# Performance work log

Measured on AMD Instinct MI355X. Metric: run time of the kernel, lower is better.

## Reference

```python
import jax, jax.numpy as jnp
import numpy as np

B, T, C = 4, 1024, 1024
HEAD_SIZE = 64
H = C // HEAD_SIZE
N_LAYER, LAYER_ID = 24, 12
D_MIX_LORA, D_DECAY_LORA = 32, 64
HEAD_SIZE_DIVISOR = 8
LN_EPS = 1e-5 * HEAD_SIZE_DIVISOR ** 2


def setup_inputs() -> dict:
    key = jax.random.key(0)
    ks = jax.random.split(key, 16)
    x = jax.random.normal(ks[0], (B, T, C), jnp.float32)

    r01 = LAYER_ID / (N_LAYER - 1)          # ratio_0_to_1
    r10 = 1.0 - LAYER_ID / N_LAYER          # ratio_1_to_almost0
    ddd = np.arange(C, dtype=np.float64) / C

    time_maa_x = jnp.asarray((1.0 - ddd ** r10).astype(np.float32))
    time_maa_w = jnp.asarray((1.0 - ddd ** r10).astype(np.float32))
    time_maa_k = jnp.asarray((1.0 - ddd ** r10).astype(np.float32))
    time_maa_v = jnp.asarray((1.0 - (ddd ** r10 + 0.3 * r01)).astype(np.float32))
    time_maa_r = jnp.asarray((1.0 - ddd ** (0.5 * r10)).astype(np.float32))
    time_maa_g = jnp.asarray((1.0 - ddd ** (0.5 * r10)).astype(np.float32))

    n = np.arange(C, dtype=np.float64)
    time_decay = jnp.asarray((-6.0 + 5.0 * (n / (C - 1)) ** (0.7 + 1.3 * r01)).astype(np.float32))
    zigzag = ((n + 1) % 3 - 1) * 0.1
    time_faaaa = jnp.asarray((r01 * (1.0 - n / (C - 1)) + zigzag).astype(np.float32)).reshape(H, HEAD_SIZE)

    u = lambda k, shp: jax.random.uniform(k, shp, jnp.float32, -0.01, 0.01)
    time_maa_w1 = u(ks[1], (C, D_MIX_LORA * 5))   # zeros in orig init; small random for a non-trivial test
    time_maa_w2 = u(ks[2], (5, D_MIX_LORA, C))
    time_decay_w1 = u(ks[3], (C, D_DECAY_LORA))
    time_decay_w2 = u(ks[4], (D_DECAY_LORA, C))

    s = 1.0 / np.sqrt(C)
    Wr = jax.random.normal(ks[5], (C, C), jnp.float32) * s   # stored [in, out]
    Wk = jax.random.normal(ks[6], (C, C), jnp.float32) * s
    Wv = jax.random.normal(ks[7], (C, C), jnp.float32) * s
    Wg = jax.random.normal(ks[8], (C, C), jnp.float32) * s
    Wo = jax.random.normal(ks[9], (C, C), jnp.float32) * s
    ln_w = jnp.ones((C,), jnp.float32)
    ln_b = jnp.zeros((C,), jnp.float32)

    return dict(x=x, time_maa_x=time_maa_x, time_maa_w=time_maa_w, time_maa_k=time_maa_k,
                time_maa_v=time_maa_v, time_maa_r=time_maa_r, time_maa_g=time_maa_g,
                time_maa_w1=time_maa_w1, time_maa_w2=time_maa_w2,
                time_decay=time_decay, time_decay_w1=time_decay_w1, time_decay_w2=time_decay_w2,
                time_faaaa=time_faaaa, Wr=Wr, Wk=Wk, Wv=Wv, Wg=Wg, Wo=Wo, ln_w=ln_w, ln_b=ln_b)


def _wkv6(r, k, v, w, u):
    # r,k,v,w: [B,T,H,N]; u: [H,N]. Data-dependent linear recurrence per head.
    def step(S, inp):               # S: [B,H,N,N] (key dim j, value dim i)
        r_t, k_t, v_t, w_t = inp    # each [B,H,N]
        y = jnp.einsum('bhj,bhji->bhi', r_t, S) \
            + jnp.sum(r_t * u * k_t, axis=-1, keepdims=True) * v_t
        decay = jnp.exp(-jnp.exp(w_t))            # CUDA kernel: w_eff = exp(-exp(w))
        S = decay[..., None] * S + k_t[..., None] * v_t[..., None, :]
        return S, y

    to_t = lambda a: jnp.transpose(a, (1, 0, 2, 3))  # [T,B,H,N]
    S0 = jnp.zeros(r.shape[:1] + (r.shape[2], r.shape[3], r.shape[3]), r.dtype)
    _, ys = jax.lax.scan(step, S0, (to_t(r), to_t(k), to_t(v), to_t(w)))
    return jnp.transpose(ys, (1, 0, 2, 3))            # [B,T,H,N]


def reference(x, time_maa_x, time_maa_w, time_maa_k, time_maa_v, time_maa_r, time_maa_g,
              time_maa_w1, time_maa_w2, time_decay, time_decay_w1, time_decay_w2,
              time_faaaa, Wr, Wk, Wv, Wg, Wo, ln_w, ln_b):
    b, t, c = x.shape
    h, n = H, HEAD_SIZE

    # token shift: ZeroPad2d((0,0,1,-1)) shifts time right by one with zero pad
    xx = jnp.concatenate([jnp.zeros_like(x[:, :1]), x[:, :-1]], axis=1) - x
    xxx = x + xx * time_maa_x
    mix = jnp.tanh(xxx @ time_maa_w1).reshape(b, t, 5, D_MIX_LORA)
    m = jnp.einsum('btsd,sdc->sbtc', mix, time_maa_w2)  # [5,B,T,C]
    xw = x + xx * (time_maa_w + m[0])
    xk = x + xx * (time_maa_k + m[1])
    xv = x + xx * (time_maa_v + m[2])
    xr = x + xx * (time_maa_r + m[3])
    xg = x + xx * (time_maa_g + m[4])

    r = xr @ Wr
    k = xk @ Wk
    v = xv @ Wv
    g = jax.nn.silu(xg @ Wg)
    w = time_decay + jnp.tanh(xw @ time_decay_w1) @ time_decay_w2

    y = _wkv6(r.reshape(b, t, h, n), k.reshape(b, t, h, n),
              v.reshape(b, t, h, n), w.reshape(b, t, h, n), time_faaaa)

    # GroupNorm with n_head groups over channel dim, eps = 1e-5 * divisor^2
    mu = y.mean(-1, keepdims=True)
    var = y.var(-1, keepdims=True)
    yn = ((y - mu) / jnp.sqrt(var + LN_EPS)).reshape(b, t, c) * ln_w + ln_b

    return (yn * g) @ Wo
```

## Files before the change

### kernel.cpp

```cpp
#include <hip/hip_runtime.h>

typedef unsigned short u16;
typedef short short8 __attribute__((ext_vector_type(8)));
typedef short short4v __attribute__((ext_vector_type(4)));
typedef float float4v __attribute__((ext_vector_type(4)));
typedef unsigned uint4v __attribute__((ext_vector_type(4)));

__device__ __forceinline__ float bf2f(u16 h) { return __uint_as_float(((unsigned)h) << 16); }
__device__ __forceinline__ u16 f2bf(float f) {
  unsigned u = __float_as_uint(f);
  unsigned r = (u + 0x7fffu + ((u >> 16) & 1u)) >> 16;
  return (u16)r;
}
__device__ __forceinline__ bool is_f32(const void* probe) {
  return ((const u16*)probe)[0] != 0x3F80;
}
__device__ __forceinline__ float ldin(const void* p, long i, bool f32m) {
  return f32m ? ((const float*)p)[i] : bf2f(((const u16*)p)[i]);
}

typedef __attribute__((address_space(1))) const unsigned int as1_u32;
typedef __attribute__((address_space(3))) unsigned int as3_u32;
__device__ __forceinline__ void gl2lds16(const void* g, void* l) {
  __builtin_amdgcn_global_load_lds((as1_u32*)g, (as3_u32*)l, 16, 0, 0);
}

template <int CTRL>
__device__ __forceinline__ float dpp_add(float x) {
  int s = __builtin_amdgcn_update_dpp(0, __float_as_int(x), CTRL, 0xF, 0xF, true);
  return x + __int_as_float(s);
}

__global__ __launch_bounds__(256) void sentinel_fill(u16* o, long n) {
  long i = (long)blockIdx.x * 256 + threadIdx.x;
  if (i < n) o[i] = 0x42C8;
}

struct TDescArr {
  const void* src[13];
  u16* dst[13];
  int rows[13];
  int cols[13];
  int roff[13];
};

__global__ __launch_bounds__(256) void transpose_all(TDescArr d, const void* probe) {
  bool f32m = is_f32(probe);
  int z = blockIdx.z;
  int rows = d.rows[z], cols = d.cols[z], roff = d.roff[z];
  int bc = blockIdx.x * 32, br = blockIdx.y * 32;
  if (bc >= cols || br >= rows) return;
  const void* src = d.src[z];
  u16* dst = d.dst[z];
  __shared__ u16 tile[32][33];
  int tx = threadIdx.x & 31, ty = threadIdx.x >> 5;
#pragma unroll
  for (int i = 0; i < 32; i += 8)
    tile[ty + i][tx] = f2bf(ldin(src, (long)(roff + br + ty + i) * cols + bc + tx, f32m));
  __syncthreads();
#pragma unroll
  for (int i = 0; i < 32; i += 8)
    dst[(long)(bc + ty + i) * rows + br + tx] = tile[tx][ty + i];
}

__global__ __launch_bounds__(256) void token_shift(const void* __restrict__ x,
                                                   const void* __restrict__ maa_x,
                                                   u16* __restrict__ xxx) {
  bool f32m = is_f32(maa_x);
  long idx = (long)blockIdx.x * 256 + threadIdx.x;
  int c = (int)(idx & 1023);
  int tt = (int)((idx >> 10) & 1023);
  float xv = ldin(x, idx, f32m);
  float xp = tt > 0 ? ldin(x, idx - 1024, f32m) : 0.f;
  xxx[idx] = f2bf(xv + (xp - xv) * ldin(maa_x, c, f32m));
}

template <int EPI>
__device__ __forceinline__ void gemm128_core(const u16* __restrict__ A,
                                             const u16* __restrict__ Bt,
                                             void* __restrict__ Cv, int N, int K,
                                             int m0, int n0, u16* As, u16* Bs,
                                             bool f32m) {
  int t = threadIdx.x, lane = t & 63, w = t >> 6;
  int wm = (w >> 1) * 64, wn = (w & 1) * 64;
  int lr = lane & 15, lk = lane >> 4;
  float4v acc[4][4];
#pragma unroll
  for (int i = 0; i < 4; i++)
#pragma unroll
    for (int j = 0; j < 4; j++) acc[i][j] = (float4v){0.f, 0.f, 0.f, 0.f};
  int srow = t >> 3;
  int scol = ((t & 7) ^ (srow & 7)) * 8;
  const u16* Ag = A + (long)(m0 + srow) * K + scol;
  const u16* Bg = Bt + (long)(n0 + srow) * K + scol;
  int so = w * 512;
  for (int k0 = 0; k0 < K; k0 += 64) {
    __syncthreads();
#pragma unroll
    for (int p = 0; p < 4; p++) {
      gl2lds16(Ag + (long)p * 32 * K + k0, As + p * 2048 + so);
      gl2lds16(Bg + (long)p * 32 * K + k0, Bs + p * 2048 + so);
    }
    __syncthreads();
    short8 af[4][2], bfr[4][2];
#pragma unroll
    for (int i = 0; i < 4; i++) {
      int R = wm + i * 16 + lr;
#pragma unroll
      for (int h = 0; h < 2; h++) {
        int j = h * 4 + lk;
        af[i][h] = *(const short8*)(As + R * 64 + (j ^ (R & 7)) * 8);
      }
    }
#pragma unroll
    for (int i = 0; i < 4; i++) {
      int R = wn + i * 16 + lr;
#pragma unroll
      for (int h = 0; h < 2; h++) {
        int j = h * 4 + lk;
        bfr[i][h] = *(const short8*)(Bs + R * 64 + (j ^ (R & 7)) * 8);
      }
    }
#pragma unroll
    for (int mi2 = 0; mi2 < 4; mi2++)
#pragma unroll
      for (int ni2 = 0; ni2 < 4; ni2++) {
        acc[mi2][ni2] = __builtin_amdgcn_mfma_f32_16x16x32_bf16(
            af[mi2][0], bfr[ni2][0], acc[mi2][ni2], 0, 0, 0);
        acc[mi2][ni2] = __builtin_amdgcn_mfma_f32_16x16x32_bf16(
            af[mi2][1], bfr[ni2][1], acc[mi2][ni2], 0, 0, 0);
      }
  }
#pragma unroll
  for (int mi2 = 0; mi2 < 4; mi2++) {
#pragma unroll
    for (int ni2 = 0; ni2 < 4; ni2++) {
      int col = n0 + wn + ni2 * 16 + lr;
#pragma unroll
      for (int rr = 0; rr < 4; rr++) {
        long row = m0 + wm + mi2 * 16 + lk * 4 + rr;
        float val = acc[mi2][ni2][rr];
        if (EPI == 1) val = val / (1.f + __expf(-val));
        if (EPI == 2 && f32m) ((float*)Cv)[row * N + col] = val;
        else ((u16*)Cv)[row * N + col] = f2bf(val);
      }
    }
  }
}

template <int EPI>
__global__ __launch_bounds__(256, 2) void gemm_big(const u16* __restrict__ A,
                                                   const u16* __restrict__ Bt,
                                                   void* __restrict__ Cv, int M, int N,
                                                   int K, const void* probe) {
  __shared__ alignas(16) u16 As[128 * 64];
  __shared__ alignas(16) u16 Bs[128 * 64];
  int sid = blockIdx.y * gridDim.x + blockIdx.x;
  int per8 = (gridDim.x * gridDim.y) >> 3;
  int L = (sid & 7) * per8 + (sid >> 3);
  int mi = L / gridDim.y, ni = L % gridDim.y;
  bool f32m = (EPI == 2) ? is_f32(probe) : false;
  gemm128_core<EPI>(A, Bt, Cv, N, K, mi * 128, ni * 128, As, Bs, f32m);
}

template <int EPI0, int EPI1>
__global__ __launch_bounds__(256, 2) void gemm_big2(
    const u16* __restrict__ A0, const u16* __restrict__ Bt0, u16* __restrict__ C0,
    const u16* __restrict__ A1, const u16* __restrict__ Bt1, u16* __restrict__ C1,
    int M, int N, int K) {
  __shared__ alignas(16) u16 As[128 * 64];
  __shared__ alignas(16) u16 Bs[128 * 64];
  int z = blockIdx.z;
  int sid = blockIdx.y * gridDim.x + blockIdx.x;
  int per8 = (gridDim.x * gridDim.y) >> 3;
  int L = (sid & 7) * per8 + (sid >> 3);
  int mi = L / gridDim.y, ni = L % gridDim.y;
  if (z == 0)
    gemm128_core<EPI0>(A0, Bt0, C0, N, K, mi * 128, ni * 128, As, Bs, false);
  else
    gemm128_core<EPI1>(A1, Bt1, C1, N, K, mi * 128, ni * 128, As, Bs, false);
}

template <int EPI>
__global__ __launch_bounds__(256) void gemm_wave(const u16* __restrict__ A, int lda,
                                                 const u16* __restrict__ Bt,
                                                 u16* __restrict__ C, int ldc,
                                                 float* dA_, float* dB_, int Ntot,
                                                 int K, const void* aux0,
                                                 const void* probe,
                                                 const void* __restrict__ xin) {
  int t = threadIdx.x, lane = t & 63, w = t >> 6;
  int m0 = blockIdx.x * 64 + w * 16;
  int span = Ntot / gridDim.y;
  int col0 = blockIdx.y * span;
  const u16* Bp = Bt + (long)col0 * K;
  int lr = lane & 15, lk = lane >> 4;
  bool f32m = (EPI >= 2) ? is_f32(probe) : false;
  int nt = span >> 4;
  for (int g0 = 0; g0 < nt; g0 += 4) {
    int gc = (nt - g0 < 4) ? (nt - g0) : 4;
    float4v acc[4];
#pragma unroll
    for (int i = 0; i < 4; i++) acc[i] = (float4v){0.f, 0.f, 0.f, 0.f};
    for (int k0 = 0; k0 < K; k0 += 32) {
      short8 a = *(const short8*)(A + (long)(m0 + lr) * lda + k0 + lk * 8);
      for (int gi = 0; gi < gc; gi++) {
        int n0 = (g0 + gi) * 16;
        short8 b = *(const short8*)(Bp + (long)(n0 + lr) * K + k0 + lk * 8);
        acc[gi] = __builtin_amdgcn_mfma_f32_16x16x32_bf16(a, b, acc[gi], 0, 0, 0);
      }
    }
    for (int gi = 0; gi < gc; gi++) {
      int col = col0 + (g0 + gi) * 16 + lr;
      if (EPI == 3) {
        long r0 = m0 + lk * 4;
        float xv4[4];
#pragma unroll
        for (int rr = 0; rr < 4; rr++)
          xv4[rr] = ldin(xin, (r0 + rr) * 1024 + col, f32m);
        float xpv = ((int)(r0 & 1023) > 0) ? ldin(xin, (r0 - 1) * 1024 + col, f32m) : 0.f;
        float mv = ldin(aux0, col, f32m);
#pragma unroll
        for (int rr = 0; rr < 4; rr++) {
          float xv = xv4[rr];
          float xp = (rr == 0) ? xpv : xv4[rr - 1];
          C[(r0 + rr) * 1024 + col] = f2bf(xv + (xp - xv) * (mv + acc[gi][rr]));
        }
      } else {
#pragma unroll
        for (int rr = 0; rr < 4; rr++) {
          long row = m0 + lk * 4 + rr;
          float val = acc[gi][rr];
          if (EPI == 0) {
            C[row * ldc + col] = f2bf(val);
          } else if (EPI == 1) {
            float vv = fminf(fmaxf(val, -15.f), 15.f);
            float e = __expf(2.f * vv);
            C[row * ldc + col] = f2bf((e - 1.f) / (e + 1.f));
          } else if (EPI == 2) {
            float wv = val + ldin(aux0, col, f32m);
            float ew = __expf(wv);
            if (row < 2048) dA_[row * 1024 + col] = ew;
            else dB_[(row - 2048) * 1024 + col] = ew;
          }
        }
      }
    }
  }
}

__global__ __launch_bounds__(256) void gemm_wave3_pair(
    const u16* __restrict__ A0, const u16* __restrict__ Bt0, u16* __restrict__ C0,
    const void* __restrict__ maa0, const u16* __restrict__ A1,
    const u16* __restrict__ Bt1, u16* __restrict__ C1,
    const void* __restrict__ maa1, const void* probe,
    const void* __restrict__ xin) {
  int z = blockIdx.z;
  const u16* A = z ? A1 : A0;
  const u16* Bt = z ? Bt1 : Bt0;
  u16* C = z ? C1 : C0;
  const void* maa = z ? maa1 : maa0;
  bool f32m = is_f32(probe);
  int t = threadIdx.x, lane = t & 63, w = t >> 6;
  int m0 = blockIdx.x * 64 + w * 16;
  int col0 = blockIdx.y * 32;
  const u16* Bp = Bt + (long)col0 * 32;
  int lr = lane & 15, lk = lane >> 4;
  float4v acc[2];
  acc[0] = (float4v){0.f, 0.f, 0.f, 0.f};
  acc[1] = (float4v){0.f, 0.f, 0.f, 0.f};
  short8 a = *(const short8*)(A + (long)(m0 + lr) * 160 + lk * 8);
#pragma unroll
  for (int gi = 0; gi < 2; gi++) {
    short8 b = *(const short8*)(Bp + (long)(gi * 16 + lr) * 32 + lk * 8);
    acc[gi] = __builtin_amdgcn_mfma_f32_16x16x32_bf16(a, b, acc[gi], 0, 0, 0);
  }
#pragma unroll
  for (int gi = 0; gi < 2; gi++) {
    int col = col0 + gi * 16 + lr;
    long r0 = m0 + lk * 4;
    float xv4[4];
#pragma unroll
    for (int rr = 0; rr < 4; rr++)
      xv4[rr] = ldin(xin, (r0 + rr) * 1024 + col, f32m);
    float xpv = ((int)(r0 & 1023) > 0) ? ldin(xin, (r0 - 1) * 1024 + col, f32m) : 0.f;
    float mv = ldin(maa, col, f32m);
#pragma unroll
    for (int rr = 0; rr < 4; rr++) {
      float xv = xv4[rr];
      float xp = (rr == 0) ? xpv : xv4[rr - 1];
      C[(r0 + rr) * 1024 + col] = f2bf(xv + (xp - xv) * (mv + acc[gi][rr]));
    }
  }
}

__global__ __launch_bounds__(256) void gemm_n64_tanh(const u16* __restrict__ A,
                                                     const u16* __restrict__ Bt,
                                                     u16* __restrict__ C) {
  int t = threadIdx.x, lane = t & 63, w = t >> 6;
  int m0 = blockIdx.x * 16;
  int n0 = w * 16;
  int lr = lane & 15, lk = lane >> 4;
  float4v acc = (float4v){0.f, 0.f, 0.f, 0.f};
  const u16* Ap = A + (long)(m0 + lr) * 1024;
  const u16* Bp = Bt + (long)(n0 + lr) * 1024;
  for (int k0 = 0; k0 < 1024; k0 += 32) {
    short8 a = *(const short8*)(Ap + k0 + lk * 8);
    short8 b = *(const short8*)(Bp + k0 + lk * 8);
    acc = __builtin_amdgcn_mfma_f32_16x16x32_bf16(a, b, acc, 0, 0, 0);
  }
#pragma unroll
  for (int rr = 0; rr < 4; rr++) {
    long row = m0 + lk * 4 + rr;
    float vv = fminf(fmaxf(acc[rr], -15.f), 15.f);
    float e = __expf(2.f * vv);
    C[row * 64 + n0 + lr] = f2bf((e - 1.f) / (e + 1.f));
  }
}

__global__ __launch_bounds__(256) void wkv6_chunk(
    const u16* __restrict__ r, const u16* __restrict__ k, const u16* __restrict__ v,
    const float* __restrict__ ewA, const float* __restrict__ ewB,
    const void* __restrict__ u_, const void* probe, u16* __restrict__ y) {
  bool f32m = is_f32(probe);
  int bx = blockIdx.x;
  int vs = bx >> 6, bh = bx & 63;
  int b = bh >> 4, h = bh & 15;
  int tid = threadIdx.x, lane = tid & 63, w = tid >> 6;
  int lr = lane & 15, lk = lane >> 4;

  __shared__ alignas(16) float raw[32][68];
  __shared__ alignas(16) float scc[2][32][68];
  __shared__ alignas(16) u16 Rp[32][72];
  __shared__ alignas(16) u16 Kp[32][72];
  __shared__ alignas(16) u16 KdF[64 * 40 + 56];
  __shared__ alignas(16) u16 Vt[32][40];
  __shared__ alignas(16) u16 Pb[32][40];
  __shared__ alignas(16) u16 Sh[32][72];
  __shared__ alignas(16) u16 Sl[32][72];
  __shared__ float diag32[32];

  const long base = ((long)b << 20) + h * 64;
  const float* ewg =
      (b < 2 ? ewA + (long)b * 1048576 : ewB + (long)(b - 2) * 1048576) + h * 64;

  int tt = tid >> 3, kg = tid & 7;
  int ck = w * 16 + (lane & 15);
  int cq = lane >> 4;
  float u8[8];
#pragma unroll
  for (int i = 0; i < 8; i++) u8[i] = ldin(u_, h * 64 + kg * 8 + i, f32m);

  float4v Sst[2];
  Sst[0] = (float4v){0.f, 0.f, 0.f, 0.f};
  Sst[1] = (float4v){0.f, 0.f, 0.f, 0.f};
  int skey = w * 16 + lk * 4;

  {
    long grow = (long)tt << 10;
    float4v ewlo = *(const float4v*)(ewg + grow + kg * 8);
    float4v ewhi = *(const float4v*)(ewg + grow + kg * 8 + 4);
    short8 rraw = *(const short8*)(r + base + grow + kg * 8);
    short8 kraw = *(const short8*)(k + base + grow + kg * 8);
    short4v vraw = *(const short4v*)(v + base + grow + vs * 32 + kg * 4);
    *(float4v*)&raw[tt][kg * 8] = ewlo;
    *(float4v*)&raw[tt][kg * 8 + 4] = ewhi;
    __syncthreads();
    {
      float pseg[8];
      float s = 0.f;
#pragma unroll
      for (int j = 0; j < 8; j++) {
        s += raw[cq * 8 + j][ck];
        pseg[j] = s;
      }
      float tot = pseg[7], x = tot;
      float up = __shfl_up(x, 16);
      if (cq >= 1) x += up;
      up = __shfl_up(x, 32);
      if (cq >= 2) x += up;
      float pre = x - tot;
#pragma unroll
      for (int j = 0; j < 8; j++) scc[0][cq * 8 + j][ck] = pre + pseg[j];
    }
    __syncthreads();
    {
      float pd = 0.f;
      short8 rpv, kpv;
#pragma unroll
      for (int i = 0; i < 8; i++) {
        int key = kg * 8 + i;
        float rf = bf2f((u16)rraw[i]);
        float kf = bf2f((u16)kraw[i]);
        float si = scc[0][tt][key];
        float sx = tt ? scc[0][tt - 1][key] : 0.f;
        float sE = scc[0][31][key];
        rpv[i] = (short)f2bf(rf * __expf(-sx));
        kpv[i] = (short)f2bf(kf * __expf(si));
        KdF[key * 40 + ((key >> 3) & 7) * 8 + tt] = f2bf(kf * __expf(si - sE));
        pd = fmaf(rf * u8[i], kf, pd);
      }
      *(short8*)&Rp[tt][kg * 8] = rpv;
      *(short8*)&Kp[tt][kg * 8] = kpv;
      pd = dpp_add<0xB1>(pd);
      pd = dpp_add<0x4E>(pd);
      pd = dpp_add<0x104>(pd);
      if (kg == 0) diag32[tt] = pd;
    }
#pragma unroll
    for (int i = 0; i < 4; i++) Vt[kg * 4 + i][tt] = (u16)vraw[i];
#pragma unroll
    for (int vt = 0; vt < 2; vt++) {
      short4v z4 = (short4v){0, 0, 0, 0};
      *(short4v*)&Sh[lr + vt * 16][skey] = z4;
      *(short4v*)&Sl[lr + vt * 16][skey] = z4;
    }
    __syncthreads();
  }

  for (int ci = 0; ci < 32; ++ci) {
    int c0 = ci << 5;
    int c0n = (ci == 31) ? c0 : c0 + 32;
    int pc = ci & 1, pn = pc ^ 1;
    long grow = (long)(c0n + tt) << 10;
    float4v ewlo = *(const float4v*)(ewg + grow + kg * 8);
    float4v ewhi = *(const float4v*)(ewg + grow + kg * 8 + 4);
    short8 rraw = *(const short8*)(r + base + grow + kg * 8);
    short8 kraw = *(const short8*)(k + base + grow + kg * 8);
    short4v vraw = *(const short4v*)(v + base + grow + vs * 32 + kg * 4);

    {
      int pt = w >> 1, pj = w & 1;
      float4v pacc = (float4v){0.f, 0.f, 0.f, 0.f};
      short8 aP0 = *(const short8*)&Rp[pt * 16 + lr][lk * 8];
      short8 aP1 = *(const short8*)&Rp[pt * 16 + lr][lk * 8 + 32];
      short8 bP0 = *(const short8*)&Kp[pj * 16 + lr][lk * 8];
      short8 bP1 = *(const short8*)&Kp[pj * 16 + lr][lk * 8 + 32];
      pacc = __builtin_amdgcn_mfma_f32_16x16x32_bf16(aP0, bP0, pacc, 0, 0, 0);
      pacc = __builtin_amdgcn_mfma_f32_16x16x32_bf16(aP1, bP1, pacc, 0, 0, 0);
      int jcol = pj * 16 + lr;
#pragma unroll
      for (int rr = 0; rr < 4; rr++) {
        int trow = pt * 16 + lk * 4 + rr;
        float val = (jcol < trow) ? pacc[rr] : (jcol == trow ? diag32[trow] : 0.f);
        Pb[trow][jcol] = f2bf(val);
      }
    }
    *(float4v*)&raw[tt][kg * 8] = ewlo;
    *(float4v*)&raw[tt][kg * 8 + 4] = ewhi;
    __syncthreads();

    {
      float pseg[8];
      float s = 0.f;
#pragma unroll
      for (int j = 0; j < 8; j++) {
        s += raw[cq * 8 + j][ck];
        pseg[j] = s;
      }
      float tot = pseg[7], x = tot;
      float up = __shfl_up(x, 16);
      if (cq >= 1) x += up;
      up = __shfl_up(x, 32);
      if (cq >= 2) x += up;
      float pre = x - tot;
#pragma unroll
      for (int j = 0; j < 8; j++) scc[pn][cq * 8 + j][ck] = pre + pseg[j];
    }
    {
      int yt = w >> 1, yv = w & 1;
      float4v yacc = (float4v){0.f, 0.f, 0.f, 0.f};
      short8 aY = *(const short8*)&Pb[yt * 16 + lr][lk * 8];
      short8 bY = *(const short8*)&Vt[yv * 16 + lr][lk * 8];
      yacc = __builtin_amdgcn_mfma_f32_16x16x32_bf16(aY, bY, yacc, 0, 0, 0);
      short8 aR0 = *(const short8*)&Rp[yt * 16 + lr][lk * 8];
      short8 aR1 = *(const short8*)&Rp[yt * 16 + lr][lk * 8 + 32];
      short8 bH0 = *(const short8*)&Sh[yv * 16 + lr][lk * 8];
      short8 bH1 = *(const short8*)&Sh[yv * 16 + lr][lk * 8 + 32];
      short8 bL0 = *(const short8*)&Sl[yv * 16 + lr][lk * 8];
      short8 bL1 = *(const short8*)&Sl[yv * 16 + lr][lk * 8 + 32];
      yacc = __builtin_amdgcn_mfma_f32_16x16x32_bf16(aR0, bH0, yacc, 0, 0, 0);
      yacc = __builtin_amdgcn_mfma_f32_16x16x32_bf16(aR1, bH1, yacc, 0, 0, 0);
      yacc = __builtin_amdgcn_mfma_f32_16x16x32_bf16(aR0, bL0, yacc, 0, 0, 0);
      yacc = __builtin_amdgcn_mfma_f32_16x16x32_bf16(aR1, bL1, yacc, 0, 0, 0);
#pragma unroll
      for (int rr = 0; rr < 4; rr++) {
        int trow = yt * 16 + lk * 4 + rr;
        y[base + ((long)(c0 + trow) << 10) + vs * 32 + yv * 16 + lr] = f2bf(yacc[rr]);
      }
      int kr = w * 16 + lr;
      short8 aS = *(const short8*)&KdF[kr * 40 + ((kr >> 3) & 7) * 8 + lk * 8];
      short8 bS0 = *(const short8*)&Vt[lr][lk * 8];
      short8 bS1 = *(const short8*)&Vt[16 + lr][lk * 8];
      float4v sa0 = (float4v){0.f, 0.f, 0.f, 0.f};
      float4v sa1 = (float4v){0.f, 0.f, 0.f, 0.f};
      sa0 = __builtin_amdgcn_mfma_f32_16x16x32_bf16(aS, bS0, sa0, 0, 0, 0);
      sa1 = __builtin_amdgcn_mfma_f32_16x16x32_bf16(aS, bS1, sa1, 0, 0, 0);
#pragma unroll
      for (int rr = 0; rr < 4; rr++) {
        float cl = __expf(-scc[pc][31][skey + rr]);
        Sst[0][rr] = fmaf(Sst[0][rr], cl, sa0[rr]);
        Sst[1][rr] = fmaf(Sst[1][rr], cl, sa1[rr]);
      }
    }
    __syncthreads();

    {
      float pd = 0.f;
      short8 rpv, kpv;
#pragma unroll
      for (int i = 0; i < 8; i++) {
        int key = kg * 8 + i;
        float rf = bf2f((u16)rraw[i]);
        float kf = bf2f((u16)kraw[i]);
        float si = scc[pn][tt][key];
        float sx = tt ? scc[pn][tt - 1][key] : 0.f;
        float sE = scc[pn][31][key];
        rpv[i] = (short)f2bf(rf * __expf(-sx));
        kpv[i] = (short)f2bf(kf * __expf(si));
        KdF[key * 40 + ((key >> 3) & 7) * 8 + tt] = f2bf(kf * __expf(si - sE));
        pd = fmaf(rf * u8[i], kf, pd);
      }
      *(short8*)&Rp[tt][kg * 8] = rpv;
      *(short8*)&Kp[tt][kg * 8] = kpv;
      pd = dpp_add<0xB1>(pd);
      pd = dpp_add<0x4E>(pd);
      pd = dpp_add<0x104>(pd);
      if (kg == 0) diag32[tt] = pd;
    }
#pragma unroll
    for (int i = 0; i < 4; i++) Vt[kg * 4 + i][tt] = (u16)vraw[i];
#pragma unroll
    for (int vt = 0; vt < 2; vt++) {
      short4v hi4, lo4;
#pragma unroll
      for (int rr = 0; rr < 4; rr++) {
        u16 hv = f2bf(Sst[vt][rr]);
        hi4[rr] = (short)hv;
        lo4[rr] = (short)f2bf(Sst[vt][rr] - bf2f(hv));
      }
      *(short4v*)&Sh[lr + vt * 16][skey] = hi4;
      *(short4v*)&Sl[lr + vt * 16][skey] = lo4;
    }
    __syncthreads();
  }
}

__global__ __launch_bounds__(256) void gn_gate(const u16* __restrict__ y,
                                               const u16* __restrict__ g,
                                               const void* __restrict__ lnw,
                                               const void* __restrict__ lnb,
                                               const void* probe,
                                               u16* __restrict__ out) {
  bool f32m = is_f32(probe);
  int gid = blockIdx.x * 4 + (threadIdx.x >> 6);
  int lane = threadIdx.x & 63;
  int h = gid & 15;
  long row = gid >> 4;
  long off = row * 1024 + h * 64 + lane;
  float val = bf2f(y[off]);
  float s = val, sq = val * val;
#pragma unroll
  for (int m = 1; m < 64; m <<= 1) {
    s += __shfl_xor(s, m);
    sq += __shfl_xor(sq, m);
  }
  float mean = s * (1.f / 64.f);
  float var = fmaxf(sq * (1.f / 64.f) - mean * mean, 0.f);
  float inv = rsqrtf(var + 6.4e-4f);
  int c = h * 64 + lane;
  float yn = (val - mean) * inv * ldin(lnw, c, f32m) + ldin(lnb, c, f32m);
  out[off] = f2bf(yn * bf2f(g[off]));
}

extern "C" void kernel_launch(void* const* d_in, const int* in_sizes, int n_in,
                              void* d_out, int out_size, void* d_ws, size_t ws_size,
                              hipStream_t stream) {
  const void* x = d_in[0];
  const void* maaX = d_in[1];
  const void* maa_s[5] = {d_in[2], d_in[3], d_in[4], d_in[5], d_in[6]};
  const void* w1 = d_in[7];
  const void* w2 = d_in[8];
  const void* tdec = d_in[9];
  const void* dw1 = d_in[10];
  const void* dw2 = d_in[11];
  const void* faaaa = d_in[12];
  const void* Wr = d_in[13];
  const void* Wk = d_in[14];
  const void* Wv = d_in[15];
  const void* Wg = d_in[16];
  const void* Wo = d_in[17];
  const void* lnw = d_in[18];
  const void* lnb = d_in[19];

  const long oWoT = 4194304;
  const long ow1T = 5242880;
  const long odw1T = 5406720;
  const long odw2T = 5472256;
  const long ow2T = 5537792;
  const long omixb = 5701632;
  const long owtan = 6356992;
  const long oxxxg = 6619136;
  const long omx = 10813440;
  const long orb = 15007744;
  const long okb = 19202048;
  const long ovb = 23396352;
  const long oyb = 27590656;
  const long oend = 31784960;
  const size_t needed = (size_t)oend * 2;

  if (ws_size < needed) {
    sentinel_fill<<<dim3((unsigned)((out_size + 255) / 256)), 256, 0, stream>>>(
        (u16*)d_out, out_size);
    return;
  }

  u16* W = (u16*)d_ws;
  u16* WrT = W;
  u16* WkT = W + 1048576;
  u16* WvT = W + 2097152;
  u16* WgT = W + 3145728;
  u16* WoT = W + oWoT;
  u16* w1T = W + ow1T;
  u16* dw1T = W + odw1T;
  u16* dw2T = W + odw2T;
  u16* w2T = W + ow2T;
  u16* mixb = W + omixb;
  u16* wtan = W + owtan;
  u16* xxxg = W + oxxxg;
  u16* mx = W + omx;
  u16* rbuf = W + orb;
  u16* kbuf = W + okb;
  u16* vbuf = W + ovb;
  u16* ybuf = W + oyb;
  float* dA_ = (float*)W;
  float* dB_ = (float*)(W + omx);
  u16* gated = mx;

  TDescArr td;
  const void* s5[5] = {Wr, Wk, Wv, Wg, Wo};
  u16* t5[5] = {WrT, WkT, WvT, WgT, WoT};
  for (int i = 0; i < 13; i++) td.roff[i] = 0;
  for (int i = 0; i < 5; i++) {
    td.src[i] = s5[i]; td.dst[i] = t5[i]; td.rows[i] = 1024; td.cols[i] = 1024;
  }
  td.src[5] = w1;  td.dst[5] = w1T;  td.rows[5] = 1024; td.cols[5] = 160;
  td.src[6] = dw1; td.dst[6] = dw1T; td.rows[6] = 1024; td.cols[6] = 64;
  td.src[7] = dw2; td.dst[7] = dw2T; td.rows[7] = 64;   td.cols[7] = 1024;
  for (int s = 0; s < 5; s++) {
    td.src[8 + s] = w2;
    td.dst[8 + s] = w2T + s * 1024 * 32;
    td.rows[8 + s] = 32; td.cols[8 + s] = 1024; td.roff[8 + s] = s * 32;
  }

  transpose_all<<<dim3(32, 32, 13), 256, 0, stream>>>(td, maaX);
  token_shift<<<dim3(16384), 256, 0, stream>>>(x, maaX, xxxg);
  gemm_wave<1><<<dim3(64, 10), 256, 0, stream>>>(xxxg, 1024, w1T, mixb, 160, nullptr,
                                                 nullptr, 160, 1024, nullptr, nullptr,
                                                 nullptr);
  gemm_wave3_pair<<<dim3(64, 32, 2), 256, 0, stream>>>(
      mixb + 3 * 32, w2T + 3 * 32768, mx, maa_s[3],
      mixb + 1 * 32, w2T + 1 * 32768, ybuf, maa_s[1], maaX, x);
  gemm_big2<0, 0><<<dim3(32, 8, 2), 256, 0, stream>>>(mx, WrT, rbuf, ybuf, WkT, kbuf,
                                                      4096, 1024, 1024);
  gemm_wave3_pair<<<dim3(64, 32, 2), 256, 0, stream>>>(
      mixb + 2 * 32, w2T + 2 * 32768, mx, maa_s[2],
      mixb + 4 * 32, w2T + 4 * 32768, ybuf, maa_s[4], maaX, x);
  gemm_big2<0, 1><<<dim3(32, 8, 2), 256, 0, stream>>>(mx, WvT, vbuf, ybuf, WgT, xxxg,
                                                      4096, 1024, 1024);
  gemm_wave<3><<<dim3(64, 32), 256, 0, stream>>>(mixb + 0 * 32, 160, w2T + 0 * 32768,
                                                 mx, 1024, nullptr, nullptr, 1024, 32,
                                                 maa_s[0], maaX, x);
  gemm_n64_tanh<<<dim3(256), 256, 0, stream>>>(mx, dw1T, wtan);
  gemm_wave<2><<<dim3(64, 16), 256, 0, stream>>>(wtan, 64, dw2T, nullptr, 0, dA_, dB_,
                                                 1024, 64, tdec, maaX, nullptr);
  wkv6_chunk<<<dim3(128), 256, 0, stream>>>(rbuf, kbuf, vbuf, dA_, dB_, faaaa, maaX,
                                            ybuf);
  gn_gate<<<dim3(16384), 256, 0, stream>>>(ybuf, xxxg, lnw, lnb, maaX, gated);
  gemm_big<2><<<dim3(32, 8), 256, 0, stream>>>(gated, WoT, d_out, 4096, 1024, 1024, maaX);
}
```

Baseline: 357.5 us.

## Merge value-split WKV6 blocks into one 512-thread block per batch-head

```diff
diff --git a/kernel.cpp b/kernel.cpp
--- a/kernel.cpp
+++ b/kernel.cpp
@@ -318,13 +318,12 @@
   }
 }
 
-__global__ __launch_bounds__(256) void wkv6_chunk(
+__global__ __launch_bounds__(512) void wkv6_chunk(
     const u16* __restrict__ r, const u16* __restrict__ k, const u16* __restrict__ v,
     const float* __restrict__ ewA, const float* __restrict__ ewB,
     const void* __restrict__ u_, const void* probe, u16* __restrict__ y) {
   bool f32m = is_f32(probe);
-  int bx = blockIdx.x;
-  int vs = bx >> 6, bh = bx & 63;
+  int bh = blockIdx.x;
   int b = bh >> 4, h = bh & 15;
   int tid = threadIdx.x, lane = tid & 63, w = tid >> 6;
   int lr = lane & 15, lk = lane >> 4;
@@ -334,39 +333,40 @@
   __shared__ alignas(16) u16 Rp[32][72];
   __shared__ alignas(16) u16 Kp[32][72];
   __shared__ alignas(16) u16 KdF[64 * 40 + 56];
-  __shared__ alignas(16) u16 Vt[32][40];
+  __shared__ alignas(16) u16 Vt[64][40];
   __shared__ alignas(16) u16 Pb[32][40];
-  __shared__ alignas(16) u16 Sh[32][72];
-  __shared__ alignas(16) u16 Sl[32][72];
+  __shared__ alignas(16) u16 Sh[64][72];
+  __shared__ alignas(16) u16 Sl[64][72];
   __shared__ float diag32[32];
 
   const long base = ((long)b << 20) + h * 64;
   const float* ewg =
       (b < 2 ? ewA + (long)b * 1048576 : ewB + (long)(b - 2) * 1048576) + h * 64;
 
-  int tt = tid >> 3, kg = tid & 7;
-  int ck = w * 16 + (lane & 15);
+  int tt = tid >> 4, kg4 = tid & 15;
+  int ck = (w & 3) * 16 + (lane & 15);
   int cq = lane >> 4;
-  float u8[8];
-#pragma unroll
-  for (int i = 0; i < 8; i++) u8[i] = ldin(u_, h * 64 + kg * 8 + i, f32m);
+  float u4[4];
+#pragma unroll
+  for (int i = 0; i < 4; i++) u4[i] = ldin(u_, h * 64 + kg4 * 4 + i, f32m);
+
+  int kw = (w & 3) * 16, vq = w >> 2;
+  int skey = kw + lk * 4;
+  int yt = w >> 2, yv = w & 3;
 
   float4v Sst[2];
   Sst[0] = (float4v){0.f, 0.f, 0.f, 0.f};
   Sst[1] = (float4v){0.f, 0.f, 0.f, 0.f};
-  int skey = w * 16 + lk * 4;
 
   {
     long grow = (long)tt << 10;
-    float4v ewlo = *(const float4v*)(ewg + grow + kg * 8);
-    float4v ewhi = *(const float4v*)(ewg + grow + kg * 8 + 4);
-    short8 rraw = *(const short8*)(r + base + grow + kg * 8);
-    short8 kraw = *(const short8*)(k + base + grow + kg * 8);
-    short4v vraw = *(const short4v*)(v + base + grow + vs * 32 + kg * 4);
-    *(float4v*)&raw[tt][kg * 8] = ewlo;
-    *(float4v*)&raw[tt][kg * 8 + 4] = ewhi;
-    __syncthreads();
-    {
+    float4v ewq = *(const float4v*)(ewg + grow + kg4 * 4);
+    short4v rraw = *(const short4v*)(r + base + grow + kg4 * 4);
+    short4v kraw = *(const short4v*)(k + base + grow + kg4 * 4);
+    short4v vraw = *(const short4v*)(v + base + grow + kg4 * 4);
+    *(float4v*)&raw[tt][kg4 * 4] = ewq;
+    __syncthreads();
+    if (w < 4) {
       float pseg[8];
       float s = 0.f;
 #pragma unroll
@@ -386,10 +386,10 @@
     __syncthreads();
     {
       float pd = 0.f;
-      short8 rpv, kpv;
-#pragma unroll
-      for (int i = 0; i < 8; i++) {
-        int key = kg * 8 + i;
+      short4v rpv, kpv;
+#pragma unroll
+      for (int i = 0; i < 4; i++) {
+        int key = kg4 * 4 + i;
         float rf = bf2f((u16)rraw[i]);
         float kf = bf2f((u16)kraw[i]);
         float si = scc[0][tt][key];
@@ -398,22 +398,23 @@
         rpv[i] = (short)f2bf(rf * __expf(-sx));
         kpv[i] = (short)f2bf(kf * __expf(si));
         KdF[key * 40 + ((key >> 3) & 7) * 8 + tt] = f2bf(kf * __expf(si - sE));
-        pd = fmaf(rf * u8[i], kf, pd);
-      }
-      *(short8*)&Rp[tt][kg * 8] = rpv;
-      *(short8*)&Kp[tt][kg * 8] = kpv;
+        pd = fmaf(rf * u4[i], kf, pd);
+      }
+      *(short4v*)&Rp[tt][kg4 * 4] = rpv;
+      *(short4v*)&Kp[tt][kg4 * 4] = kpv;
       pd = dpp_add<0xB1>(pd);
       pd = dpp_add<0x4E>(pd);
       pd = dpp_add<0x104>(pd);
-      if (kg == 0) diag32[tt] = pd;
-    }
-#pragma unroll
-    for (int i = 0; i < 4; i++) Vt[kg * 4 + i][tt] = (u16)vraw[i];
+      pd = dpp_add<0x108>(pd);
+      if (kg4 == 0) diag32[tt] = pd;
+    }
+#pragma unroll
+    for (int i = 0; i < 4; i++) Vt[kg4 * 4 + i][tt] = (u16)vraw[i];
 #pragma unroll
     for (int vt = 0; vt < 2; vt++) {
       short4v z4 = (short4v){0, 0, 0, 0};
-      *(short4v*)&Sh[lr + vt * 16][skey] = z4;
-      *(short4v*)&Sl[lr + vt * 16][skey] = z4;
+      *(short4v*)&Sh[vq * 32 + vt * 16 + lr][skey] = z4;
+      *(short4v*)&Sl[vq * 32 + vt * 16 + lr][skey] = z4;
     }
     __syncthreads();
   }
@@ -423,13 +424,12 @@
     int c0n = (ci == 31) ? c0 : c0 + 32;
     int pc = ci & 1, pn = pc ^ 1;
     long grow = (long)(c0n + tt) << 10;
-    float4v ewlo = *(const float4v*)(ewg + grow + kg * 8);
-    float4v ewhi = *(const float4v*)(ewg + grow + kg * 8 + 4);
-    short8 rraw = *(const short8*)(r + base + grow + kg * 8);
-    short8 kraw = *(const short8*)(k + base + grow + kg * 8);
-    short4v vraw = *(const short4v*)(v + base + grow + vs * 32 + kg * 4);
-
-    {
+    float4v ewq = *(const float4v*)(ewg + grow + kg4 * 4);
+    short4v rraw = *(const short4v*)(r + base + grow + kg4 * 4);
+    short4v kraw = *(const short4v*)(k + base + grow + kg4 * 4);
+    short4v vraw = *(const short4v*)(v + base + grow + kg4 * 4);
+
+    if (w < 4) {
       int pt = w >> 1, pj = w & 1;
       float4v pacc = (float4v){0.f, 0.f, 0.f, 0.f};
       short8 aP0 = *(const short8*)&Rp[pt * 16 + lr][lk * 8];
@@ -446,11 +446,10 @@
         Pb[trow][jcol] = f2bf(val);
       }
     }
-    *(float4v*)&raw[tt][kg * 8] = ewlo;
-    *(float4v*)&raw[tt][kg * 8 + 4] = ewhi;
-    __syncthreads();
-
-    {
+    *(float4v*)&raw[tt][kg4 * 4] = ewq;
+    __syncthreads();
+
+    if (w < 4) {
       float pseg[8];
       float s = 0.f;
 #pragma unroll
@@ -468,7 +467,6 @@
       for (int j = 0; j < 8; j++) scc[pn][cq * 8 + j][ck] = pre + pseg[j];
     }
     {
-      int yt = w >> 1, yv = w & 1;
       float4v yacc = (float4v){0.f, 0.f, 0.f, 0.f};
       short8 aY = *(const short8*)&Pb[yt * 16 + lr][lk * 8];
       short8 bY = *(const short8*)&Vt[yv * 16 + lr][lk * 8];
@@ -486,12 +484,12 @@
 #pragma unroll
       for (int rr = 0; rr < 4; rr++) {
         int trow = yt * 16 + lk * 4 + rr;
-        y[base + ((long)(c0 + trow) << 10) + vs * 32 + yv * 16 + lr] = f2bf(yacc[rr]);
-      }
-      int kr = w * 16 + lr;
+        y[base + ((long)(c0 + trow) << 10) + yv * 16 + lr] = f2bf(yacc[rr]);
+      }
+      int kr = kw + lr;
       short8 aS = *(const short8*)&KdF[kr * 40 + ((kr >> 3) & 7) * 8 + lk * 8];
-      short8 bS0 = *(const short8*)&Vt[lr][lk * 8];
-      short8 bS1 = *(const short8*)&Vt[16 + lr][lk * 8];
+      short8 bS0 = *(const short8*)&Vt[vq * 32 + lr][lk * 8];
+      short8 bS1 = *(const short8*)&Vt[vq * 32 + 16 + lr][lk * 8];
       float4v sa0 = (float4v){0.f, 0.f, 0.f, 0.f};
       float4v sa1 = (float4v){0.f, 0.f, 0.f, 0.f};
       sa0 = __builtin_amdgcn_mfma_f32_16x16x32_bf16(aS, bS0, sa0, 0, 0, 0);
@@ -507,10 +505,10 @@
 
     {
       float pd = 0.f;
-      short8 rpv, kpv;
-#pragma unroll
-      for (int i = 0; i < 8; i++) {
-        int key = kg * 8 + i;
+      short4v rpv, kpv;
+#pragma unroll
+      for (int i = 0; i < 4; i++) {
+        int key = kg4 * 4 + i;
         float rf = bf2f((u16)rraw[i]);
         float kf = bf2f((u16)kraw[i]);
         float si = scc[pn][tt][key];
@@ -519,17 +517,18 @@
         rpv[i] = (short)f2bf(rf * __expf(-sx));
         kpv[i] = (short)f2bf(kf * __expf(si));
         KdF[key * 40 + ((key >> 3) & 7) * 8 + tt] = f2bf(kf * __expf(si - sE));
-        pd = fmaf(rf * u8[i], kf, pd);
-      }
-      *(short8*)&Rp[tt][kg * 8] = rpv;
-      *(short8*)&Kp[tt][kg * 8] = kpv;
+        pd = fmaf(rf * u4[i], kf, pd);
+      }
+      *(short4v*)&Rp[tt][kg4 * 4] = rpv;
+      *(short4v*)&Kp[tt][kg4 * 4] = kpv;
       pd = dpp_add<0xB1>(pd);
       pd = dpp_add<0x4E>(pd);
       pd = dpp_add<0x104>(pd);
-      if (kg == 0) diag32[tt] = pd;
-    }
-#pragma unroll
-    for (int i = 0; i < 4; i++) Vt[kg * 4 + i][tt] = (u16)vraw[i];
+      pd = dpp_add<0x108>(pd);
+      if (kg4 == 0) diag32[tt] = pd;
+    }
+#pragma unroll
+    for (int i = 0; i < 4; i++) Vt[kg4 * 4 + i][tt] = (u16)vraw[i];
 #pragma unroll
     for (int vt = 0; vt < 2; vt++) {
       short4v hi4, lo4;
@@ -539,8 +538,8 @@
         hi4[rr] = (short)hv;
         lo4[rr] = (short)f2bf(Sst[vt][rr] - bf2f(hv));
       }
-      *(short4v*)&Sh[lr + vt * 16][skey] = hi4;
-      *(short4v*)&Sl[lr + vt * 16][skey] = lo4;
+      *(short4v*)&Sh[vq * 32 + vt * 16 + lr][skey] = hi4;
+      *(short4v*)&Sl[vq * 32 + vt * 16 + lr][skey] = lo4;
     }
     __syncthreads();
   }
@@ -674,8 +673,8 @@
   gemm_n64_tanh<<<dim3(256), 256, 0, stream>>>(mx, dw1T, wtan);
   gemm_wave<2><<<dim3(64, 16), 256, 0, stream>>>(wtan, 64, dw2T, nullptr, 0, dA_, dB_,
                                                  1024, 64, tdec, maaX, nullptr);
-  wkv6_chunk<<<dim3(128), 256, 0, stream>>>(rbuf, kbuf, vbuf, dA_, dB_, faaaa, maaX,
-                                            ybuf);
+  wkv6_chunk<<<dim3(64), 512, 0, stream>>>(rbuf, kbuf, vbuf, dA_, dB_, faaaa, maaX,
+                                           ybuf);
   gn_gate<<<dim3(16384), 256, 0, stream>>>(ybuf, xxxg, lnw, lnb, maaX, gated);
   gemm_big<2><<<dim3(32, 8), 256, 0, stream>>>(gated, WoT, d_out, 4096, 1024, 1024, maaX);
 }
```

Result: no change. 353.5 us (-1.1%).
